# Performance work log

Measured on AMD Instinct MI355X. Metric: run time of the kernel, lower is better.

The kernel has to match this reference:

```python
import jax, jax.numpy as jnp
import numpy as np
from jax import lax

# NOTE: ResidualConvBlock and SS2DChanelFirst are reconstructed from the repo's
# conventions: ResidualConvBlock = act(conv3x3 -> act -> conv3x3 + 1x1 skip);
# SS2DChanelFirst = standard VMamba SS2D (in_proj -> dw-conv3x3 -> SiLU ->
# 4-direction cross-scan selective scan -> cross-merge -> LayerNorm -> *SiLU(z)
# gate -> out_proj) operating on NCHW tensors.

B, CIN, H, W = 4, 6, 64, 64
DM, DI, K, N, R, NL, GROUPS = 72, 144, 4, 8, 4, 2, 12


def conv2d(x, w, b=None, groups=1):
    out = lax.conv_general_dilated(x, w, (1, 1), 'SAME',
                                   dimension_numbers=('NCHW', 'OIHW', 'NCHW'),
                                   feature_group_count=groups)
    if b is not None:
        out = out + b[None, :, None, None]
    return out


def lrelu(x, s):
    return jnp.where(x >= 0, x, s * x)


def selective_scan(u, delta, A, Bs, Cs, D):
    # u, delta: (b,K,C,L); A: (K,C,N); Bs, Cs: (b,K,N,L); D: (K,C)
    b, k, c, l = u.shape
    n = A.shape[-1]
    ul = jnp.moveaxis(u, -1, 0)
    dl = jnp.moveaxis(delta, -1, 0)
    Bl = jnp.moveaxis(Bs, -1, 0)
    Cl = jnp.moveaxis(Cs, -1, 0)
    h0 = jnp.zeros((b, k, c, n), u.dtype)

    def step(h, xt):
        d_t, u_t, B_t, C_t = xt
        h = h * jnp.exp(d_t[..., None] * A) + (d_t * u_t)[..., None] * B_t[:, :, None, :]
        return h, jnp.einsum('bkcn,bkn->bkc', h, C_t)

    _, ys = lax.scan(step, h0, (dl, ul, Bl, Cl))
    return jnp.moveaxis(ys, 0, -1) + u * D[None, :, :, None]


def ss2d(x, in_w, dw_w, dw_b, xp_w, dtp_w, dtp_b, A_logs, Ds, ong, onb, op_w):
    b, dm, h_, w_ = x.shape
    l = h_ * w_
    xz = jnp.einsum('ec,bchw->behw', in_w, x)  # (b, 2*DI, h, w)
    xi, z = xz[:, :DI], xz[:, DI:]
    xi = jax.nn.silu(conv2d(xi, dw_w, dw_b, groups=DI))
    # cross-scan: row-major, col-major, and their reverses
    x0 = xi.reshape(b, DI, l)
    x1 = jnp.swapaxes(xi, 2, 3).reshape(b, DI, l)
    xs = jnp.stack([x0, x1, x0[..., ::-1], x1[..., ::-1]], axis=1)  # (b,4,DI,l)
    x_dbl = jnp.einsum('bkdl,kcd->bkcl', xs, xp_w)  # (b,4,R+2N,l)
    dts, Bs, Cs = x_dbl[:, :, :R], x_dbl[:, :, R:R + N], x_dbl[:, :, R + N:]
    dts = jnp.einsum('bkrl,kdr->bkdl', dts, dtp_w)
    delta = jax.nn.softplus(dts + dtp_b[None, :, :, None])
    A = -jnp.exp(A_logs).reshape(K, DI, N)
    ys = selective_scan(xs, delta, A, Bs, Cs, Ds.reshape(K, DI))  # (b,4,DI,l)
    # cross-merge
    y = ys[:, 0] + ys[:, 2, :, ::-1]
    yt = ys[:, 1] + ys[:, 3, :, ::-1]
    y = y + jnp.swapaxes(yt.reshape(b, DI, w_, h_), 2, 3).reshape(b, DI, l)
    y = jnp.swapaxes(y, 1, 2)  # (b,l,DI)
    mu = y.mean(-1, keepdims=True)
    var = ((y - mu) ** 2).mean(-1, keepdims=True)
    y = (y - mu) / jnp.sqrt(var + 1e-5) * ong + onb
    y = y * jax.nn.silu(jnp.swapaxes(z.reshape(b, DI, l), 1, 2))
    out = jnp.einsum('bld,ed->ble', y, op_w)  # (b,l,DM)
    return jnp.swapaxes(out, 1, 2).reshape(b, dm, h_, w_)


def groupnorm(x, g, bta, groups):
    b, c, h_, w_ = x.shape
    xg = x.reshape(b, groups, c // groups, h_ * w_)
    mu = xg.mean((2, 3), keepdims=True)
    var = ((xg - mu) ** 2).mean((2, 3), keepdims=True)
    xg = (xg - mu) / jnp.sqrt(var + 1e-5)
    return xg.reshape(b, c, h_, w_) * g[None, :, None, None] + bta[None, :, None, None]


def setup_inputs() -> dict:
    key = jax.random.key(0)
    ks = iter(jax.random.split(key, 32))
    nrm = lambda shp, s=0.05: jax.random.normal(next(ks), shp, jnp.float32) * s
    inp = {
        'image': jax.random.normal(next(ks), (B, CIN, H, W), jnp.float32),
        'cb_w1': nrm((DM, CIN, 3, 3), 0.1), 'cb_b1': nrm((DM,), 0.02),
        'cb_w2': nrm((DM, DM, 3, 3), 0.05), 'cb_b2': nrm((DM,), 0.02),
        'cb_ws': nrm((DM, CIN, 1, 1), 0.1), 'cb_bs': nrm((DM,), 0.02),
        'in_w': nrm((NL, 2 * DI, DM), 0.05),
        'dw_w': nrm((NL, DI, 1, 3, 3), 0.1), 'dw_b': nrm((NL, DI), 0.02),
        'xp_w': nrm((NL, K, R + 2 * N, DI), 0.05),
        'dtp_w': nrm((NL, K, DI, R), 0.1), 'dtp_b': nrm((NL, K, DI), 0.1),
        'A_logs': nrm((NL, K * DI, N), 0.5),
        'Ds': jnp.ones((NL, K * DI), jnp.float32) + nrm((NL, K * DI), 0.05),
        'ong': jnp.ones((NL, DI), jnp.float32), 'onb': jnp.zeros((NL, DI), jnp.float32),
        'op_w': nrm((NL, DM, DI), 0.05),
        'gn_g': jnp.ones((NL, DM), jnp.float32), 'gn_b': jnp.zeros((NL, DM), jnp.float32),
        'l1_w': nrm((NL, DM, DM), 0.1), 'l1_b': nrm((NL, DM), 0.02),
        'l2_w': nrm((NL, DM, DM), 0.1), 'l2_b': nrm((NL, DM), 0.02),
        'shrink_w': nrm((CIN, DM, 3, 3), 0.05), 'shrink_b': nrm((CIN,), 0.02),
    }
    return inp


def reference(image, cb_w1, cb_b1, cb_w2, cb_b2, cb_ws, cb_bs, in_w, dw_w, dw_b,
              xp_w, dtp_w, dtp_b, A_logs, Ds, ong, onb, op_w, gn_g, gn_b,
              l1_w, l1_b, l2_w, l2_b, shrink_w, shrink_b):
    # ResidualConvBlock (expand 6 -> 72), leaky_relu
    h = lrelu(conv2d(image, cb_w1, cb_b1), 0.01)
    h = conv2d(h, cb_w2, cb_b2) + conv2d(image, cb_ws, cb_bs)
    x = lrelu(h, 0.01)
    for i in range(NL):
        x = ss2d(x, in_w[i], dw_w[i], dw_b[i], xp_w[i], dtp_w[i], dtp_b[i],
                 A_logs[i], Ds[i], ong[i], onb[i], op_w[i])
        x = groupnorm(x, gn_g[i], gn_b[i], GROUPS)
        x = jnp.einsum('oc,bchw->bohw', l1_w[i], x) + l1_b[i][None, :, None, None]
        x = lrelu(x, 0.04)
        x = jnp.einsum('oc,bchw->bohw', l2_w[i], x) + l2_b[i][None, :, None, None]
    x = conv2d(x, shrink_w, shrink_b)
    return jax.nn.sigmoid(x)
```

## Files before the change

kernel.cpp:

```cpp
#include <hip/hip_runtime.h>
#include <math.h>

#define BB 4
#define CI 6
#define LL 4096
#define DMC 72
#define DIC 144
#define KD 4
#define NS 8
#define RD 4
#define NLAYER 2
#define GRP 12
#define NCH 256
#define TS 16
#define SP 72
#define PPN (66*SP)
#define L2E 1.4426950408889634f

__device__ __forceinline__ float sigmoidf_(float x){ return 1.f/(1.f+__expf(-x)); }
__device__ __forceinline__ float siluf_(float x){ return x*sigmoidf_(x); }
__device__ __forceinline__ float softplusf_(float x){
  return fmaxf(x,0.f) + __logf(1.f + __expf(-fabsf(x)));
}

__device__ __forceinline__ int padidx(int p){ return SP*(p>>6) + (p&63) + SP + 4; }

#define LOAD9(ip, a) do { \
  a[0]=(ip)[-SP-1]; a[1]=(ip)[-SP]; a[2]=(ip)[-SP+1]; \
  a[3]=(ip)[-1];    a[4]=(ip)[0];   a[5]=(ip)[1];     \
  a[6]=(ip)[SP-1];  a[7]=(ip)[SP];  a[8]=(ip)[SP+1];  } while(0)

__device__ __forceinline__ void load6(const float* __restrict__ base, float v[6]){
  v[0] = base[-1];
  float4 f = *(const float4*)base;
  v[1]=f.x; v[2]=f.y; v[3]=f.z; v[4]=f.w;
  v[5] = base[4];
}

__global__ void k_halo(float* __restrict__ pads, int nplanes){
  int plane = blockIdx.x;
  if (plane >= nplanes) return;
  int t = threadIdx.x;
  if (t >= 260) return;
  float* pl = pads + (size_t)plane*PPN;
  int row, col;
  if (t < 132){
    row = (t < 66) ? 0 : 65;
    col = 3 + (t % 66);
  } else {
    int j = t - 132;
    col = (j < 64) ? 3 : 68;
    row = 1 + (j & 63);
  }
  pl[row*SP + col] = 0.f;
}

__global__ void k_pad_img(const float* __restrict__ img, float* __restrict__ img_pad){
  int idx = blockIdx.x*256 + threadIdx.x;
  if (idx >= BB*CI*LL) return;
  int p = idx & 4095; int bc = idx >> 12;
  img_pad[(size_t)bc*PPN + padidx(p)] = img[idx];
}

__global__ void k_conv1(const float* __restrict__ img_pad, const float* __restrict__ w,
                        const float* __restrict__ bias, float* __restrict__ tmp_pad){
  int bid = blockIdx.x;
  int tile = bid & 3; int r = bid >> 2; int o = r % DMC; int b = r / DMC;
  int p0 = tile*1024 + threadIdx.x*4;
  int pb = padidx(p0);
  float bv = bias[o];
  float acc[4] = {bv,bv,bv,bv};
  #pragma unroll
  for (int ic=0; ic<CI; ++ic){
    const float* ip = img_pad + (size_t)(b*CI+ic)*PPN + pb;
    const float* wr = w + (o*CI+ic)*9;
    #pragma unroll
    for (int rr=0; rr<3; ++rr){
      float v[6]; load6(ip + (rr-1)*SP, v);
      float w0=wr[rr*3], w1=wr[rr*3+1], w2v=wr[rr*3+2];
      #pragma unroll
      for (int q=0;q<4;++q) acc[q] += v[q]*w0 + v[q+1]*w1 + v[q+2]*w2v;
    }
  }
  #pragma unroll
  for (int q=0;q<4;++q) acc[q] = acc[q] >= 0.f ? acc[q] : 0.01f*acc[q];
  *(float4*)(tmp_pad + (size_t)(b*DMC+o)*PPN + pb) = make_float4(acc[0],acc[1],acc[2],acc[3]);
}

__global__ void k_conv2init(const float* __restrict__ img, const float* __restrict__ b2,
                            const float* __restrict__ wsc, const float* __restrict__ bsc,
                            float* __restrict__ xout){
  int bid = blockIdx.x;
  int t = bid & 15; int r = bid >> 4; int og = r % 18; int b = r / 18;
  int p = t*256 + threadIdx.x;
  float acc[4];
  #pragma unroll
  for (int j=0;j<4;++j) acc[j] = b2[og*4+j] + bsc[og*4+j];
  #pragma unroll
  for (int ic=0; ic<CI; ++ic){
    float v = img[((b*CI+ic)<<12)+p];
    #pragma unroll
    for (int j=0;j<4;++j) acc[j] += v * wsc[(og*4+j)*CI+ic];
  }
  #pragma unroll
  for (int j=0;j<4;++j)
    xout[((b*DMC+og*4+j)<<12)+p] = acc[j];
}

__global__ void k_conv2(const float* __restrict__ tmp_pad,
                        const float* __restrict__ w2, float* __restrict__ xout){
  int bid = blockIdx.x;
  int t = bid & 15; int r = bid >> 4; int og = r % 18; r /= 18;
  int icg = r & 1; int b = r >> 1;
  int p = t*256 + threadIdx.x;
  int pb = padidx(p);
  float acc[4] = {0.f,0.f,0.f,0.f};
  const float* ipb = tmp_pad + (size_t)b*DMC*PPN + pb;
  const float* wb  = w2 + (size_t)(og*4)*DMC*9;
  #pragma unroll 2
  for (int ii=0; ii<36; ++ii){
    int ic = icg*36 + ii;
    const float* ip = ipb + (size_t)ic*PPN;
    float a[9]; LOAD9(ip, a);
    const float* wp = wb + ic*9;
    #pragma unroll
    for (int j=0;j<4;++j){
      float s = 0.f;
      #pragma unroll
      for (int q=0;q<9;++q) s += a[q]*wp[(size_t)j*DMC*9 + q];
      acc[j] += s;
    }
  }
  #pragma unroll
  for (int j=0;j<4;++j)
    atomicAdd(xout + ((b*DMC+og*4+j)<<12)+p, acc[j]);
}

__global__ void k_xz(const float* __restrict__ x, const float* __restrict__ inw,
                     float* __restrict__ xz_pad, float* __restrict__ z_t, int relu){
  int bid = blockIdx.x;
  int t = bid & 15; int r = bid >> 4; int eg = r % 36; int b = r / 36;
  int p = t*256 + threadIdx.x;
  float acc[8] = {0.f,0.f,0.f,0.f,0.f,0.f,0.f,0.f};
  for (int c0=0; c0<DMC; c0+=4){
    float a[4];
    #pragma unroll
    for (int q=0;q<4;++q) a[q] = x[((b*DMC+c0+q)<<12)+p];
    if (relu){
      #pragma unroll
      for (int q=0;q<4;++q) a[q] = a[q] >= 0.f ? a[q] : 0.01f*a[q];
    }
    #pragma unroll
    for (int j=0;j<8;++j){
      float4 w = *(const float4*)(inw + (eg*8+j)*DMC + c0);
      acc[j] += a[0]*w.x + a[1]*w.y + a[2]*w.z + a[3]*w.w;
    }
  }
  if (eg < 18){
    int pb = padidx(p);
    #pragma unroll
    for (int j=0;j<8;++j) xz_pad[(size_t)(b*DIC+eg*8+j)*PPN + pb] = acc[j];
  } else {
    float* zb = z_t + ((size_t)b*LL+p)*DIC + (eg*8-DIC);
    *(float4*)(zb)   = make_float4(acc[0],acc[1],acc[2],acc[3]);
    *(float4*)(zb+4) = make_float4(acc[4],acc[5],acc[6],acc[7]);
  }
}

__global__ void k_dw(const float* __restrict__ xz_pad, const float* __restrict__ dww,
                     const float* __restrict__ dwb, float* __restrict__ xi_t){
  int bid = blockIdx.x;
  int tile = bid & 3; int r = bid >> 2; int c = r % DIC; int b = r / DIC;
  int p0 = tile*1024 + threadIdx.x*4;
  int pb = padidx(p0);
  const float* ip = xz_pad + (size_t)(b*DIC+c)*PPN + pb;
  const float* wp = dww + c*9;
  float bv = dwb[c];
  float acc[4] = {bv,bv,bv,bv};
  #pragma unroll
  for (int rr=0; rr<3; ++rr){
    float v[6]; load6(ip + (rr-1)*SP, v);
    float w0=wp[rr*3], w1=wp[rr*3+1], w2v=wp[rr*3+2];
    #pragma unroll
    for (int q=0;q<4;++q) acc[q] += v[q]*w0 + v[q+1]*w1 + v[q+2]*w2v;
  }
  #pragma unroll
  for (int q=0;q<4;++q)
    xi_t[((size_t)b*LL+p0+q)*DIC + c] = siluf_(acc[q]);
}

__global__ void k_xdbl(const float* __restrict__ xi_t, const float* __restrict__ xpw,
                       float* __restrict__ xdbl){
  int bid = blockIdx.x;
  int t = bid & 15; int r = bid >> 4;
  int kk = r & 3; r >>= 2; int part = r & 3; int b = r >> 2;
  int p = t*256 + threadIdx.x;
  const float* xib = xi_t + ((size_t)b*LL + p)*DIC;
  const float* wk = xpw + (size_t)(kk*20 + part*5)*DIC;
  float acc[5] = {0.f,0.f,0.f,0.f,0.f};
  for (int d=0; d<DIC; d+=4){
    float4 v = *(const float4*)(xib + d);
    #pragma unroll
    for (int c=0;c<5;++c){
      float4 w = *(const float4*)(wk + (size_t)c*DIC + d);
      acc[c] += v.x*w.x + v.y*w.y + v.z*w.z + v.w*w.w;
    }
  }
  float* dst = xdbl + ((size_t)(b*KD+kk)*LL + p)*20 + part*5;
  #pragma unroll
  for (int c=0;c<5;++c) dst[c] = acc[c];
}

__device__ __forceinline__ void scan_decode(int idx, int& b, int& k, int& ch, int& c){
  c = idx % DIC;
  int r = idx / DIC;
  ch = r % NCH;
  r /= NCH;
  k = r & 3; b = r >> 2;
}

__device__ __forceinline__ void scan_affine(int k, int ch, int& ps0, int& sk){
  int l0 = ch*TS;
  if (k == 0){ ps0 = l0; sk = 1; }
  else if (k == 1){ ps0 = ((l0 & 63) << 6) | (l0 >> 6); sk = 64; }
  else if (k == 2){ ps0 = (LL-1) - l0; sk = -1; }
  else { int m0 = (LL-1) - l0; ps0 = ((m0 & 63) << 6) | (m0 >> 6); sk = -64; }
}

__global__ void k_p1(const float* __restrict__ xi_t, const float* __restrict__ xdbl,
                     const float* __restrict__ dtpw, const float* __restrict__ dtpb,
                     const float* __restrict__ alog,
                     float* __restrict__ cumA, float* __restrict__ hp){
  int idx = blockIdx.x*256 + threadIdx.x;
  if (idx >= BB*KD*NCH*DIC) return;
  int b,k,ch,c; scan_decode(idx,b,k,ch,c);
  float Arow[NS];
  #pragma unroll
  for (int n=0;n<NS;++n) Arow[n] = -__expf(alog[(k*DIC+c)*NS+n]) * L2E;
  float4 wdt = *(const float4*)(dtpw + (k*DIC+c)*RD);
  float bdt = dtpb[k*DIC+c];
  int ps0, sk; scan_affine(k, ch, ps0, sk);
  const float* row = xdbl + (size_t)(b*KD+k)*LL*20 + (size_t)ps0*20;
  const float* up  = xi_t + (size_t)b*LL*DIC + c + (size_t)ps0*DIC;
  long rstep = (long)sk*20;
  long ustep = (long)sk*DIC;
  float h[NS];
  #pragma unroll
  for (int n=0;n<NS;++n) h[n]=0.f;
  float sumd = 0.f;
  #pragma unroll 4
  for (int t=0; t<TS; ++t){
    float4 q0 = *(const float4*)(row);
    float4 q1 = *(const float4*)(row+4);
    float4 q2 = *(const float4*)(row+8);
    float u = *up;
    float dt = bdt + q0.x*wdt.x + q0.y*wdt.y + q0.z*wdt.z + q0.w*wdt.w;
    dt = softplusf_(dt);
    sumd += dt;
    float du = dt*u;
    float Bv[NS] = {q1.x,q1.y,q1.z,q1.w,q2.x,q2.y,q2.z,q2.w};
    #pragma unroll
    for (int n=0;n<NS;++n)
      h[n] = h[n]*exp2f(dt*Arow[n]) + du*Bv[n];
    row += rstep; up += ustep;
  }
  size_t base = ((size_t)((b*KD+k)*NCH + ch)*NS)*DIC + c;
  #pragma unroll
  for (int n=0;n<NS;++n) hp[base + n*DIC] = h[n];
  #pragma unroll
  for (int n=0;n<NS;++n) cumA[base + n*DIC] = exp2f(sumd*Arow[n]);
}

__global__ void k_p2(float* __restrict__ cumA, float* __restrict__ hp,
                     float* __restrict__ gnstats){
  if (blockIdx.x == 0 && threadIdx.x < 2*BB*GRP) gnstats[threadIdx.x] = 0.f;
  int idx = blockIdx.x*256 + threadIdx.x;
  if (idx >= BB*KD*NS*DIC) return;
  int c = idx % DIC; int n = (idx/DIC) % NS; int bk = idx/(DIC*NS);
  float h = 0.f;
  #pragma unroll 8
  for (int ch=0; ch<NCH; ++ch){
    size_t base = ((size_t)(bk*NCH+ch)*NS + n)*DIC + c;
    float a = cumA[base];
    float pp = hp[base];
    cumA[base] = 0.f;
    hp[base] = h;
    h = a*h + pp;
  }
}

__global__ void k_p3(const float* __restrict__ xi_t, const float* __restrict__ xdbl,
                     const float* __restrict__ dtpw, const float* __restrict__ dtpb,
                     const float* __restrict__ alog, const float* __restrict__ Dsv,
                     const float* __restrict__ hin, float* __restrict__ y_t){
  int idx = blockIdx.x*256 + threadIdx.x;
  if (idx >= BB*KD*NCH*DIC) return;
  int b,k,ch,c; scan_decode(idx,b,k,ch,c);
  float Arow[NS];
  #pragma unroll
  for (int n=0;n<NS;++n) Arow[n] = -__expf(alog[(k*DIC+c)*NS+n]) * L2E;
  float4 wdt = *(const float4*)(dtpw + (k*DIC+c)*RD);
  float bdt = dtpb[k*DIC+c];
  float Dv = Dsv[k*DIC+c];
  int ps0, sk; scan_affine(k, ch, ps0, sk);
  const float* row = xdbl + (size_t)(b*KD+k)*LL*20 + (size_t)ps0*20;
  const float* up  = xi_t + (size_t)b*LL*DIC + c + (size_t)ps0*DIC;
  float* yp        = y_t  + (size_t)b*LL*DIC + c + (size_t)ps0*DIC;
  long rstep = (long)sk*20;
  long ustep = (long)sk*DIC;
  float h[NS];
  size_t base = ((size_t)((b*KD+k)*NCH + ch)*NS)*DIC + c;
  #pragma unroll
  for (int n=0;n<NS;++n) h[n] = hin[base + n*DIC];
  #pragma unroll 4
  for (int t=0; t<TS; ++t){
    float4 q0 = *(const float4*)(row);
    float4 q1 = *(const float4*)(row+4);
    float4 q2 = *(const float4*)(row+8);
    float4 q3 = *(const float4*)(row+12);
    float4 q4 = *(const float4*)(row+16);
    float u = *up;
    float dt = bdt + q0.x*wdt.x + q0.y*wdt.y + q0.z*wdt.z + q0.w*wdt.w;
    dt = softplusf_(dt);
    float du = dt*u;
    float Bv[NS] = {q1.x,q1.y,q1.z,q1.w,q2.x,q2.y,q2.z,q2.w};
    float Cv[NS] = {q3.x,q3.y,q3.z,q3.w,q4.x,q4.y,q4.z,q4.w};
    float y = 0.f;
    #pragma unroll
    for (int n=0;n<NS;++n){
      h[n] = h[n]*exp2f(dt*Arow[n]) + du*Bv[n];
      y += h[n]*Cv[n];
    }
    y += u*Dv;
    atomicAdd(yp, y);
    row += rstep; up += ustep; yp += ustep;
  }
}

__global__ void k_oproj(const float* __restrict__ y_t, const float* __restrict__ z_t,
                        const float* __restrict__ ong, const float* __restrict__ onb,
                        const float* __restrict__ opw, float* __restrict__ xout,
                        float* __restrict__ gnstats){
  __shared__ float ly[DIC*65];
  __shared__ float red1[8][64], red2[8][64];
  __shared__ float lmu[64], lrs[64];
  int bid = blockIdx.x;
  int tile = bid & 63; int b = bid >> 6;
  int pstart = tile*64;
  const float* src = y_t + ((size_t)b*LL + pstart)*DIC;
  for (int i = threadIdx.x; i < 64*DIC; i += 512){
    int px = i / DIC; int d = i - px*DIC;
    ly[d*65 + px] = src[i];
  }
  __syncthreads();
  int px = threadIdx.x & 63;
  int grp = threadIdx.x >> 6;
  {
    float s=0.f, q=0.f;
    for (int d=grp*18; d<grp*18+18; ++d){
      float v = ly[d*65+px]; s += v; q += v*v;
    }
    red1[grp][px]=s; red2[grp][px]=q;
  }
  __syncthreads();
  if (grp == 0){
    float st=0.f, qt=0.f;
    #pragma unroll
    for (int g=0;g<8;++g){ st += red1[g][px]; qt += red2[g][px]; }
    float mu = st*(1.f/DIC);
    float var = qt*(1.f/DIC) - mu*mu;
    lmu[px] = mu;
    lrs[px] = rsqrtf(var + 1e-5f);
  }
  __syncthreads();
  const float* zsrc = z_t + ((size_t)b*LL + pstart)*DIC;
  for (int i = threadIdx.x; i < 64*DIC; i += 512){
    int ppx = i / DIC; int d = i - ppx*DIC;
    float zv = zsrc[i];
    float v = ly[d*65+ppx];
    ly[d*65+ppx] = ((v - lmu[ppx])*lrs[ppx]*ong[d] + onb[d]) * siluf_(zv);
  }
  __syncthreads();
  int ocg = __builtin_amdgcn_readfirstlane(grp);
  float acc[9];
  #pragma unroll
  for (int j=0;j<9;++j) acc[j]=0.f;
  const float* wb = opw + (size_t)ocg*9*DIC;
  #pragma unroll 4
  for (int d=0; d<DIC; ++d){
    float a = ly[d*65 + px];
    #pragma unroll
    for (int j=0;j<9;++j) acc[j] += a * wb[(size_t)j*DIC + d];
  }
  #pragma unroll
  for (int j=0;j<9;++j)
    xout[((size_t)(b*DMC + ocg*9 + j)<<12) + pstart + px] = acc[j];
  int c0 = ocg*9;
  int gA = c0/6;
  int nA = 6 - (c0 - gA*6);
  float sA=0.f,qA=0.f,sB=0.f,qB=0.f;
  #pragma unroll
  for (int j=0;j<9;++j){
    float v = acc[j];
    if (j < nA){ sA += v; qA += v*v; } else { sB += v; qB += v*v; }
  }
  #pragma unroll
  for (int o=32; o>0; o>>=1){
    sA += __shfl_xor(sA,o,64); qA += __shfl_xor(qA,o,64);
    sB += __shfl_xor(sB,o,64); qB += __shfl_xor(qB,o,64);
  }
  if ((threadIdx.x & 63) == 0){
    atomicAdd(gnstats + (b*GRP+gA)*2,     sA);
    atomicAdd(gnstats + (b*GRP+gA)*2 + 1, qA);
    atomicAdd(gnstats + (b*GRP+gA+1)*2,     sB);
    atomicAdd(gnstats + (b*GRP+gA+1)*2 + 1, qB);
  }
}

__global__ void k_dense1(const float* __restrict__ xin, const float* __restrict__ gnstats,
                         const float* __restrict__ gng, const float* __restrict__ gnb,
                         const float* __restrict__ w, const float* __restrict__ bias,
                         float* __restrict__ xout){
  __shared__ float As[DMC], Bs[DMC];
  int bid = blockIdx.x;
  int t = bid & 15; int r = bid >> 4; int eg = r % 18; int b = r / 18;
  if (threadIdx.x < DMC){
    int c = threadIdx.x; int gr = c/6;
    float s = gnstats[(b*GRP+gr)*2];
    float q = gnstats[(b*GRP+gr)*2 + 1];
    const float inv = 1.f/(6.f*LL);
    float mu = s*inv;
    float var = q*inv - mu*mu;
    float rs = rsqrtf(var + 1e-5f);
    float A = rs*gng[c];
    As[c] = A;
    Bs[c] = gnb[c] - mu*A;
  }
  __syncthreads();
  int p = t*256 + threadIdx.x;
  float acc[4];
  #pragma unroll
  for (int j=0;j<4;++j) acc[j] = bias[eg*4+j];
  for (int c0=0; c0<DMC; c0+=4){
    float a[4];
    #pragma unroll
    for (int q=0;q<4;++q){
      float v = xin[((size_t)(b*DMC+c0+q)<<12)+p];
      a[q] = v*As[c0+q] + Bs[c0+q];
    }
    #pragma unroll
    for (int j=0;j<4;++j){
      float4 w0 = *(const float4*)(w + (eg*4+j)*DMC + c0);
      acc[j] += a[0]*w0.x + a[1]*w0.y + a[2]*w0.z + a[3]*w0.w;
    }
  }
  #pragma unroll
  for (int j=0;j<4;++j)
    xout[((size_t)(b*DMC+eg*4+j)<<12)+p] = acc[j];
}

__global__ void k_dense2(const float* __restrict__ xin, const float* __restrict__ w,
                         const float* __restrict__ bias, float* __restrict__ xout,
                         float* __restrict__ pad_out){
  int bid = blockIdx.x;
  int t = bid & 15; int r = bid >> 4; int eg = r % 18; int b = r / 18;
  int p = t*256 + threadIdx.x;
  float acc[4];
  #pragma unroll
  for (int j=0;j<4;++j) acc[j] = bias[eg*4+j];
  for (int c0=0; c0<DMC; c0+=4){
    float a[4];
    #pragma unroll
    for (int q=0;q<4;++q){
      float v = xin[((size_t)(b*DMC+c0+q)<<12)+p];
      a[q] = v >= 0.f ? v : 0.04f*v;
    }
    #pragma unroll
    for (int j=0;j<4;++j){
      float4 w0 = *(const float4*)(w + (eg*4+j)*DMC + c0);
      acc[j] += a[0]*w0.x + a[1]*w0.y + a[2]*w0.z + a[3]*w0.w;
    }
  }
  int pb = padidx(p);
  #pragma unroll
  for (int j=0;j<4;++j){
    xout[((size_t)(b*DMC+eg*4+j)<<12)+p] = acc[j];
    if (pad_out) pad_out[(size_t)(b*DMC+eg*4+j)*PPN + pb] = acc[j];
  }
}

__global__ void k_shrinkA(const float* __restrict__ x_pad, const float* __restrict__ w,
                          float* __restrict__ pacc){
  int bid = blockIdx.x;
  int t = bid & 15; int r = bid >> 4; int icg = r % 24; int b = r / 24;
  int p = t*256 + threadIdx.x;
  int pb = padidx(p);
  float acc[6] = {0.f,0.f,0.f,0.f,0.f,0.f};
  const float* ipb = x_pad + (size_t)b*DMC*PPN + pb;
  #pragma unroll
  for (int ii=0; ii<3; ++ii){
    int ic = icg*3 + ii;
    const float* ip = ipb + (size_t)ic*PPN;
    float a[9]; LOAD9(ip, a);
    #pragma unroll
    for (int o=0;o<6;++o){
      const float* wp = w + (o*DMC+ic)*9;
      float s = 0.f;
      #pragma unroll
      for (int q=0;q<9;++q) s += a[q]*wp[q];
      acc[o] += s;
    }
  }
  #pragma unroll
  for (int o=0;o<6;++o)
    atomicAdd(pacc + ((size_t)(b*CI+o)<<12)+p, acc[o]);
}

__global__ void k_sig(const float* __restrict__ pacc, const float* __restrict__ bias,
                      float* __restrict__ out){
  int idx = blockIdx.x*256 + threadIdx.x;
  if (idx >= BB*CI*LL) return;
  int o = (idx>>12) % CI;
  out[idx] = sigmoidf_(pacc[idx] + bias[o]);
}

extern "C" void kernel_launch(void* const* d_in, const int* in_sizes, int n_in,
                              void* d_out, int out_size, void* d_ws, size_t ws_size,
                              hipStream_t stream){
  const float* image = (const float*)d_in[0];
  const float* cb_w1 = (const float*)d_in[1];
  const float* cb_b1 = (const float*)d_in[2];
  const float* cb_w2 = (const float*)d_in[3];
  const float* cb_b2 = (const float*)d_in[4];
  const float* cb_ws = (const float*)d_in[5];
  const float* cb_bs = (const float*)d_in[6];
  const float* in_w  = (const float*)d_in[7];
  const float* dw_w  = (const float*)d_in[8];
  const float* dw_b  = (const float*)d_in[9];
  const float* xp_w  = (const float*)d_in[10];
  const float* dtp_w = (const float*)d_in[11];
  const float* dtp_b = (const float*)d_in[12];
  const float* A_logs= (const float*)d_in[13];
  const float* Ds    = (const float*)d_in[14];
  const float* ong   = (const float*)d_in[15];
  const float* onb   = (const float*)d_in[16];
  const float* op_w  = (const float*)d_in[17];
  const float* gn_g  = (const float*)d_in[18];
  const float* gn_b  = (const float*)d_in[19];
  const float* l1_w  = (const float*)d_in[20];
  const float* l1_b  = (const float*)d_in[21];
  const float* l2_w  = (const float*)d_in[22];
  const float* l2_b  = (const float*)d_in[23];
  const float* sh_w  = (const float*)d_in[24];
  const float* sh_b  = (const float*)d_in[25];

  const size_t SZ_X  = (size_t)BB*DMC*LL;
  const size_t SZ_C  = (size_t)BB*DIC*LL;
  const size_t SZ_XD = (size_t)BB*KD*20*LL;
  const size_t SZ_HP = (size_t)BB*KD*NCH*NS*DIC;
  const size_t SZ_IP = (size_t)BB*CI*PPN;
  const size_t SZ_TP = (size_t)BB*DMC*PPN;
  const size_t SZ_ZP = (size_t)BB*DIC*PPN;

  float* ws = (float*)d_ws;
  size_t off = 0;
  float* x     = ws + off; off += SZ_X;
  float* tmp   = ws + off; off += SZ_X;
  float* z_t   = ws + off; off += SZ_C;
  float* xi_t  = ws + off; off += SZ_C;
  float* xdbl  = ws + off; off += SZ_XD;
  float* cumA  = ws + off; off += SZ_HP;
  float* hp    = ws + off; off += SZ_HP;
  float* pads  = ws + off;
  float* img_pad = pads;
  float* tmp_pad = img_pad + SZ_IP;
  float* xz_pad  = tmp_pad + SZ_TP;
  off += SZ_IP + SZ_TP + SZ_ZP;
  float* gnstats = ws + off; off += 2*BB*GRP;
  if (ws_size < off*sizeof(float)) return;
  float* y_t = cumA;

  dim3 blk(256);
  const int NPLANES = BB*CI + BB*DMC + BB*DIC;

  k_halo<<<dim3(NPLANES), blk, 0, stream>>>(pads, NPLANES);
  k_pad_img<<<dim3(BB*CI*16), blk, 0, stream>>>(image, img_pad);
  k_conv1<<<dim3(BB*DMC*4), blk, 0, stream>>>(img_pad, cb_w1, cb_b1, tmp_pad);
  k_conv2init<<<dim3(BB*18*16), blk, 0, stream>>>(image, cb_b2, cb_ws, cb_bs, x);
  k_conv2<<<dim3(BB*2*18*16), blk, 0, stream>>>(tmp_pad, cb_w2, x);

  for (int i=0; i<NLAYER; ++i){
    const float* in_w_i  = in_w  + (size_t)i*2*DIC*DMC;
    const float* dw_w_i  = dw_w  + (size_t)i*DIC*9;
    const float* dw_b_i  = dw_b  + (size_t)i*DIC;
    const float* xp_w_i  = xp_w  + (size_t)i*KD*20*DIC;
    const float* dtp_w_i = dtp_w + (size_t)i*KD*DIC*RD;
    const float* dtp_b_i = dtp_b + (size_t)i*KD*DIC;
    const float* alog_i  = A_logs+ (size_t)i*KD*DIC*NS;
    const float* Ds_i    = Ds    + (size_t)i*KD*DIC;
    const float* ong_i   = ong   + (size_t)i*DIC;
    const float* onb_i   = onb   + (size_t)i*DIC;
    const float* op_w_i  = op_w  + (size_t)i*DMC*DIC;
    const float* gn_g_i  = gn_g  + (size_t)i*DMC;
    const float* gn_b_i  = gn_b  + (size_t)i*DMC;
    const float* l1_w_i  = l1_w  + (size_t)i*DMC*DMC;
    const float* l1_b_i  = l1_b  + (size_t)i*DMC;
    const float* l2_w_i  = l2_w  + (size_t)i*DMC*DMC;
    const float* l2_b_i  = l2_b  + (size_t)i*DMC;

    k_xz  <<<dim3(BB*36*16), blk, 0, stream>>>(x, in_w_i, xz_pad, z_t, (i==0)?1:0);
    k_dw  <<<dim3(BB*DIC*4), blk, 0, stream>>>(xz_pad, dw_w_i, dw_b_i, xi_t);
    k_xdbl<<<dim3(BB*4*KD*16), blk, 0, stream>>>(xi_t, xp_w_i, xdbl);
    k_p1  <<<dim3(BB*KD*NCH*DIC/256), blk, 0, stream>>>(xi_t, xdbl, dtp_w_i, dtp_b_i, alog_i, cumA, hp);
    k_p2  <<<dim3(BB*KD*NS*DIC/256), blk, 0, stream>>>(cumA, hp, gnstats);
    k_p3  <<<dim3(BB*KD*NCH*DIC/256), blk, 0, stream>>>(xi_t, xdbl, dtp_w_i, dtp_b_i, alog_i, Ds_i, hp, y_t);
    k_oproj<<<dim3(BB*64), dim3(512), 0, stream>>>(y_t, z_t, ong_i, onb_i, op_w_i, x, gnstats);
    k_dense1<<<dim3(BB*18*16), blk, 0, stream>>>(x, gnstats, gn_g_i, gn_b_i, l1_w_i, l1_b_i, tmp);
    k_dense2<<<dim3(BB*18*16), blk, 0, stream>>>(tmp, l2_w_i, l2_b_i, x,
                                                 (i==NLAYER-1) ? tmp_pad : (float*)nullptr);
  }

  hipMemsetAsync(tmp, 0, (size_t)BB*CI*LL*sizeof(float), stream);
  k_shrinkA<<<dim3(BB*24*16), blk, 0, stream>>>(tmp_pad, sh_w, tmp);
  k_sig<<<dim3((BB*CI*LL+255)/256), blk, 0, stream>>>(tmp, sh_b, (float*)d_out);
}
```

Baseline: 535.6 us.

## Split out-proj into LayerNorm-gate kernel and finer-grained projection kernel

The fused LayerNorm+gate+out_proj kernel, which used only 256 blocks of 512 threads with a large LDS transpose, is split in two. A new wavefront-per-pixel kernel does LayerNorm and the SiLU(z) gate in place. A new projection kernel launches 1152 blocks where each thread computes 4 output channels using float4 loads along the channel dimension. This raises parallelism and occupancy, at the cost of an extra global round trip of y_t and a strided per-thread read pattern that gives uncoalesced loads in the projection.

New measurement: 592.7 us. 1.11x slower.

```diff
diff --git a/kernel.cpp b/kernel.cpp
--- a/kernel.cpp
+++ b/kernel.cpp
@@ -337,70 +337,57 @@
   }
 }
 
-__global__ void k_oproj(const float* __restrict__ y_t, const float* __restrict__ z_t,
-                        const float* __restrict__ ong, const float* __restrict__ onb,
-                        const float* __restrict__ opw, float* __restrict__ xout,
-                        float* __restrict__ gnstats){
-  __shared__ float ly[DIC*65];
-  __shared__ float red1[8][64], red2[8][64];
-  __shared__ float lmu[64], lrs[64];
-  int bid = blockIdx.x;
-  int tile = bid & 63; int b = bid >> 6;
-  int pstart = tile*64;
-  const float* src = y_t + ((size_t)b*LL + pstart)*DIC;
-  for (int i = threadIdx.x; i < 64*DIC; i += 512){
-    int px = i / DIC; int d = i - px*DIC;
-    ly[d*65 + px] = src[i];
-  }
-  __syncthreads();
-  int px = threadIdx.x & 63;
-  int grp = threadIdx.x >> 6;
-  {
-    float s=0.f, q=0.f;
-    for (int d=grp*18; d<grp*18+18; ++d){
-      float v = ly[d*65+px]; s += v; q += v*v;
-    }
-    red1[grp][px]=s; red2[grp][px]=q;
-  }
-  __syncthreads();
-  if (grp == 0){
-    float st=0.f, qt=0.f;
-    #pragma unroll
-    for (int g=0;g<8;++g){ st += red1[g][px]; qt += red2[g][px]; }
-    float mu = st*(1.f/DIC);
-    float var = qt*(1.f/DIC) - mu*mu;
-    lmu[px] = mu;
-    lrs[px] = rsqrtf(var + 1e-5f);
-  }
-  __syncthreads();
-  const float* zsrc = z_t + ((size_t)b*LL + pstart)*DIC;
-  for (int i = threadIdx.x; i < 64*DIC; i += 512){
-    int ppx = i / DIC; int d = i - ppx*DIC;
-    float zv = zsrc[i];
-    float v = ly[d*65+ppx];
-    ly[d*65+ppx] = ((v - lmu[ppx])*lrs[ppx]*ong[d] + onb[d]) * siluf_(zv);
-  }
-  __syncthreads();
-  int ocg = __builtin_amdgcn_readfirstlane(grp);
-  float acc[9];
-  #pragma unroll
-  for (int j=0;j<9;++j) acc[j]=0.f;
-  const float* wb = opw + (size_t)ocg*9*DIC;
-  #pragma unroll 4
-  for (int d=0; d<DIC; ++d){
-    float a = ly[d*65 + px];
-    #pragma unroll
-    for (int j=0;j<9;++j) acc[j] += a * wb[(size_t)j*DIC + d];
-  }
-  #pragma unroll
-  for (int j=0;j<9;++j)
-    xout[((size_t)(b*DMC + ocg*9 + j)<<12) + pstart + px] = acc[j];
-  int c0 = ocg*9;
+__global__ void k_lnz(float* __restrict__ y_t, const float* __restrict__ z_t,
+                      const float* __restrict__ ong, const float* __restrict__ onb){
+  int gid = blockIdx.x*256 + threadIdx.x;
+  int wid = gid >> 6;
+  int lane = gid & 63;
+  if (wid >= BB*LL) return;
+  size_t rb = (size_t)wid * DIC;
+  float v0 = y_t[rb + lane];
+  float v1 = y_t[rb + 64 + lane];
+  float v2 = (lane < 16) ? y_t[rb + 128 + lane] : 0.f;
+  float s = v0 + v1 + v2;
+  float q = v0*v0 + v1*v1 + v2*v2;
+  #pragma unroll
+  for (int o=32; o>0; o>>=1){ s += __shfl_xor(s,o,64); q += __shfl_xor(q,o,64); }
+  float mu = s*(1.f/DIC);
+  float var = q*(1.f/DIC) - mu*mu;
+  float rs = rsqrtf(var + 1e-5f);
+  float z0 = z_t[rb + lane];
+  y_t[rb + lane] = ((v0-mu)*rs*ong[lane] + onb[lane]) * siluf_(z0);
+  float z1 = z_t[rb + 64 + lane];
+  y_t[rb + 64 + lane] = ((v1-mu)*rs*ong[64+lane] + onb[64+lane]) * siluf_(z1);
+  if (lane < 16){
+    float z2 = z_t[rb + 128 + lane];
+    y_t[rb + 128 + lane] = ((v2-mu)*rs*ong[128+lane] + onb[128+lane]) * siluf_(z2);
+  }
+}
+
+__global__ void k_oproj(const float* __restrict__ yn, const float* __restrict__ opw,
+                        float* __restrict__ xout, float* __restrict__ gnstats){
+  int bid = blockIdx.x;
+  int t = bid & 15; int r = bid >> 4; int og = r % 18; int b = r / 18;
+  int p = t*256 + threadIdx.x;
+  const float* yb = yn + ((size_t)b*LL + p)*DIC;
+  float acc[4] = {0.f,0.f,0.f,0.f};
+  for (int d=0; d<DIC; d+=4){
+    float4 v = *(const float4*)(yb + d);
+    #pragma unroll
+    for (int j=0;j<4;++j){
+      float4 w = *(const float4*)(opw + (og*4+j)*DIC + d);
+      acc[j] += v.x*w.x + v.y*w.y + v.z*w.z + v.w*w.w;
+    }
+  }
+  #pragma unroll
+  for (int j=0;j<4;++j)
+    xout[((size_t)(b*DMC+og*4+j)<<12)+p] = acc[j];
+  int c0 = og*4;
   int gA = c0/6;
   int nA = 6 - (c0 - gA*6);
   float sA=0.f,qA=0.f,sB=0.f,qB=0.f;
   #pragma unroll
-  for (int j=0;j<9;++j){
+  for (int j=0;j<4;++j){
     float v = acc[j];
     if (j < nA){ sA += v; qA += v*v; } else { sB += v; qB += v*v; }
   }
@@ -412,8 +399,10 @@
   if ((threadIdx.x & 63) == 0){
     atomicAdd(gnstats + (b*GRP+gA)*2,     sA);
     atomicAdd(gnstats + (b*GRP+gA)*2 + 1, qA);
-    atomicAdd(gnstats + (b*GRP+gA+1)*2,     sB);
-    atomicAdd(gnstats + (b*GRP+gA+1)*2 + 1, qB);
+    if (nA < 4){
+      atomicAdd(gnstats + (b*GRP+gA+1)*2,     sB);
+      atomicAdd(gnstats + (b*GRP+gA+1)*2 + 1, qB);
+    }
   }
 }
 
@@ -614,7 +603,8 @@
     k_p1  <<<dim3(BB*KD*NCH*DIC/256), blk, 0, stream>>>(xi_t, xdbl, dtp_w_i, dtp_b_i, alog_i, cumA, hp);
     k_p2  <<<dim3(BB*KD*NS*DIC/256), blk, 0, stream>>>(cumA, hp, gnstats);
     k_p3  <<<dim3(BB*KD*NCH*DIC/256), blk, 0, stream>>>(xi_t, xdbl, dtp_w_i, dtp_b_i, alog_i, Ds_i, hp, y_t);
-    k_oproj<<<dim3(BB*64), dim3(512), 0, stream>>>(y_t, z_t, ong_i, onb_i, op_w_i, x, gnstats);
+    k_lnz <<<dim3(BB*LL/4), blk, 0, stream>>>(y_t, z_t, ong_i, onb_i);
+    k_oproj<<<dim3(BB*18*16), blk, 0, stream>>>(y_t, op_w_i, x, gnstats);
     k_dense1<<<dim3(BB*18*16), blk, 0, stream>>>(x, gnstats, gn_g_i, gn_b_i, l1_w_i, l1_b_i, tmp);
     k_dense2<<<dim3(BB*18*16), blk, 0, stream>>>(tmp, l2_w_i, l2_b_i, x,
                                                  (i==NLAYER-1) ? tmp_pad : (float*)nullptr);
```
